# Kernel optimization log

Measured on AMD Instinct MI355X. Metric: run time of the kernel, lower is better.

Reference implementation:

```python
import jax, jax.numpy as jnp
import numpy as np

N_NODES = 100000
N_EDGES = 1600000
IN_FEAT = 128
HIDDEN = 64
OUT_EMB = 64
N_GRAPHS = 256
PD_EPS = 1e-6  # torch PairwiseDistance eps added to the difference


def gcn_conv(x, src, dst, W, b):
    """PyG GCNConv: h = x@W, add self-loops, sym-normalized scatter-add, + bias."""
    n = x.shape[0]
    h = x @ W  # [N, out]
    loops = jnp.arange(n)
    s = jnp.concatenate([src, loops])
    d = jnp.concatenate([dst, loops])
    deg = jnp.zeros((n,), h.dtype).at[d].add(1.0)
    dinv = jnp.where(deg > 0, jax.lax.rsqrt(jnp.maximum(deg, 1.0)), 0.0)
    norm = (dinv[s] * dinv[d])[:, None]  # [E+N, 1]
    out = jnp.zeros_like(h).at[d].add(norm * h[s])  # gather + scatter-add
    return out + b


def mean_pool(x, batch, num_graphs):
    s = jax.ops.segment_sum(x, batch, num_segments=num_graphs)
    cnt = jax.ops.segment_sum(jnp.ones((x.shape[0],), x.dtype), batch,
                              num_segments=num_graphs)
    return s / jnp.maximum(cnt, 1.0)[:, None]


def tower(x, edge_index, batch, params, num_graphs):
    W1, b1, W2, b2, W3, b3, Wlin, blin = params
    src, dst = edge_index[0], edge_index[1]
    x = jax.nn.relu(gcn_conv(x, src, dst, W1, b1))
    x = jax.nn.relu(gcn_conv(x, src, dst, W2, b2))
    x = gcn_conv(x, src, dst, W3, b3)
    x = mean_pool(x, batch, num_graphs)
    # dropout omitted for determinism (eval mode)
    return x @ Wlin + blin


def setup_inputs() -> dict:
    key = jax.random.key(0)
    ks = jax.random.split(key, 16)

    def glorot(k, fan_in, fan_out):
        lim = np.sqrt(6.0 / (fan_in + fan_out))
        return jax.random.uniform(k, (fan_in, fan_out), jnp.float32, -lim, lim)

    return {
        "x1": jax.random.normal(ks[0], (N_NODES, IN_FEAT), jnp.float32),
        "edge_index1": jax.random.randint(ks[1], (2, N_EDGES), 0, N_NODES),
        "batch1": jnp.sort(jax.random.randint(ks[2], (N_NODES,), 0, N_GRAPHS)),
        "x2": jax.random.normal(ks[3], (N_NODES, IN_FEAT), jnp.float32),
        "edge_index2": jax.random.randint(ks[4], (2, N_EDGES), 0, N_NODES),
        "batch2": jnp.sort(jax.random.randint(ks[5], (N_NODES,), 0, N_GRAPHS)),
        "W1": glorot(ks[6], IN_FEAT, HIDDEN),
        "b1": jnp.zeros((HIDDEN,), jnp.float32),
        "W2": glorot(ks[7], HIDDEN, HIDDEN),
        "b2": jnp.zeros((HIDDEN,), jnp.float32),
        "W3": glorot(ks[8], HIDDEN, HIDDEN),
        "b3": jnp.zeros((HIDDEN,), jnp.float32),
        "Wlin": glorot(ks[9], HIDDEN, OUT_EMB),
        "blin": jnp.zeros((OUT_EMB,), jnp.float32),
        "num_graphs": N_GRAPHS,
    }


def reference(x1, edge_index1, batch1, x2, edge_index2, batch2,
              W1, b1, W2, b2, W3, b3, Wlin, blin, num_graphs):
    params = (W1, b1, W2, b2, W3, b3, Wlin, blin)
    e1 = tower(x1, edge_index1, batch1, params, num_graphs)  # [G, OUT_EMB]
    e2 = tower(x2, edge_index2, batch2, params, num_graphs)
    diff = e1 - e2 + PD_EPS
    return jnp.sqrt(jnp.sum(diff * diff, axis=-1))  # L2 PairwiseDistance, [G]
```

## Files before the change

### kernel.cpp

```cpp
#include <hip/hip_runtime.h>
#include <hip/hip_bf16.h>
#include <math.h>

#define NGRAPHS 256
#define PD_EPS 1e-6f
#define POOL_CHUNK 64
#define NCOLOR 16
#define CSHIFT 4
#define KB 96

typedef __hip_bfloat16 bf16;
typedef unsigned short ushort_t;
typedef short bf8_t __attribute__((ext_vector_type(8)));
typedef float f4_t __attribute__((ext_vector_type(4)));

static __device__ __forceinline__ int wave_uniform(int v) {
  return __builtin_amdgcn_readfirstlane(v);
}
static __device__ __forceinline__ float b2f(bf16 h) { return __bfloat162float(h); }
static __device__ __forceinline__ bf16 f2b(float f) { return __float2bfloat16(f); }
static __device__ __forceinline__ short f2bbits(float f) {
  bf16 h = __float2bfloat16(f);
  return *reinterpret_cast<short*>(&h);
}

__global__ __launch_bounds__(256) void k_count_part(const int* __restrict__ dst,
                                                    ushort_t* __restrict__ partial,
                                                    int E, int n, int rng) {
  extern __shared__ int hist[];
  int color = blockIdx.x & (NCOLOR - 1);
  int sub = blockIdx.x >> CSHIFT;
  int base = color * rng;
  int hi = n - base; if (hi > rng) hi = rng;
  for (int i = threadIdx.x; i < rng; i += 256) hist[i] = 0;
  __syncthreads();
  const int stride = KB * 256;
  int e = sub * 256 + threadIdx.x;
  for (; e + 7 * stride < E; e += 8 * stride) {
    int d[8];
#pragma unroll
    for (int k = 0; k < 8; ++k) d[k] = dst[e + k * stride] - base;
#pragma unroll
    for (int k = 0; k < 8; ++k)
      if ((unsigned)d[k] < (unsigned)hi) atomicAdd(&hist[d[k]], 1);
  }
  for (; e < E; e += stride) {
    int d = dst[e] - base;
    if ((unsigned)d < (unsigned)hi) atomicAdd(&hist[d], 1);
  }
  __syncthreads();
  ushort_t* outp = partial + (size_t)blockIdx.x * rng;
  for (int i = threadIdx.x; i < rng; i += 256) outp[i] = (ushort_t)hist[i];
}

__global__ void k_reduce_part(ushort_t* __restrict__ partial, int* __restrict__ cnt,
                              float* __restrict__ dinv, int n, int rng) {
  int i = blockIdx.x * 256 + threadIdx.x;
  if (i >= n) return;
  int c = i / rng, li = i - c * rng;
  int acc = 0;
  for (int s = 0; s < KB; ++s) {
    size_t idx = (size_t)(s * NCOLOR + c) * rng + li;
    int t = partial[idx];
    partial[idx] = (ushort_t)acc;
    acc += t;
  }
  cnt[i] = acc;
  dinv[i] = 1.0f / sqrtf((float)(acc + 1));
}

__global__ void k_scan1(const int* __restrict__ cnt, int* __restrict__ off,
                        int* __restrict__ bsums, int n) {
  __shared__ int s[256];
  int tid = threadIdx.x;
  int gid = blockIdx.x * 256 + tid;
  int v = (gid < n) ? cnt[gid] : 0;
  s[tid] = v; __syncthreads();
  for (int o = 1; o < 256; o <<= 1) {
    int t = (tid >= o) ? s[tid - o] : 0;
    __syncthreads();
    s[tid] += t;
    __syncthreads();
  }
  if (gid < n) off[gid] = s[tid] - v;
  if (tid == 255) bsums[blockIdx.x] = s[255];
}

__global__ void k_scan2(int* __restrict__ bsums, int nb) {
  __shared__ int s[512];
  int tid = threadIdx.x;
  int v = (tid < nb) ? bsums[tid] : 0;
  s[tid] = v; __syncthreads();
  for (int o = 1; o < 512; o <<= 1) {
    int t = (tid >= o) ? s[tid - o] : 0;
    __syncthreads();
    s[tid] += t;
    __syncthreads();
  }
  if (tid < nb) bsums[tid] = s[tid] - v;
}

__global__ void k_off_final(int* __restrict__ off, const int* __restrict__ bsums,
                            int n, int E) {
  int gid = blockIdx.x * 256 + threadIdx.x;
  if (gid < n) off[gid] += bsums[blockIdx.x];
  if (gid == 0) off[n] = E;
}

__global__ __launch_bounds__(256) void k_fill_col(const int* __restrict__ src,
                                                  const int* __restrict__ dst,
                                                  const int* __restrict__ off,
                                                  const ushort_t* __restrict__ partial,
                                                  int* __restrict__ csr, int E, int n,
                                                  int rng) {
  extern __shared__ int cur[];
  int color = blockIdx.x & (NCOLOR - 1);
  int sub = blockIdx.x >> CSHIFT;
  int base = color * rng;
  int hi = n - base; if (hi > rng) hi = rng;
  const ushort_t* pp = partial + (size_t)blockIdx.x * rng;
  for (int i = threadIdx.x; i < hi; i += 256) cur[i] = off[base + i] + (int)pp[i];
  __syncthreads();
  const int stride = KB * 256;
  int e = sub * 256 + threadIdx.x;
  for (; e + 7 * stride < E; e += 8 * stride) {
    int d[8], s[8];
#pragma unroll
    for (int k = 0; k < 8; ++k) d[k] = dst[e + k * stride] - base;
#pragma unroll
    for (int k = 0; k < 8; ++k) s[k] = src[e + k * stride];
#pragma unroll
    for (int k = 0; k < 8; ++k) {
      if ((unsigned)d[k] < (unsigned)hi) {
        int p = atomicAdd(&cur[d[k]], 1);
        csr[p] = s[k];
      }
    }
  }
  for (; e < E; e += stride) {
    int d = dst[e] - base;
    if ((unsigned)d < (unsigned)hi) {
      int p = atomicAdd(&cur[d], 1);
      csr[p] = src[e];
    }
  }
}

template <int K, int INF32>
__global__ __launch_bounds__(256, 2) void k_gemm_mfma(const void* __restrict__ inv,
                                                      const float* __restrict__ Wg,
                                                      const float* __restrict__ dinv,
                                                      bf16* __restrict__ out, int n) {
  constexpr int KS = K / 32;
  int lane = threadIdx.x & 63;
  int quad = lane >> 4;
  int col = lane & 15;

  bf8_t bfrag[4][KS];
#pragma unroll
  for (int c = 0; c < 4; ++c)
#pragma unroll
    for (int s = 0; s < KS; ++s)
#pragma unroll
      for (int j = 0; j < 8; ++j)
        bfrag[c][s][j] = f2bbits(Wg[(s * 32 + quad * 8 + j) * 64 + c * 16 + col]);

  int wid = (blockIdx.x * blockDim.x + threadIdx.x) >> 6;
  int nw = (gridDim.x * blockDim.x) >> 6;
  int tiles = (n + 15) >> 4;
  for (int t = wid; t < tiles; t += nw) {
    int base = t << 4;
    int arow = base + col;
    if (arow >= n) arow = n - 1;

    bf8_t afrag[KS];
    if (INF32) {
      const float* xr = (const float*)inv + (size_t)arow * K;
#pragma unroll
      for (int s = 0; s < KS; ++s) {
        float4 u0 = *(const float4*)(xr + s * 32 + quad * 8);
        float4 u1 = *(const float4*)(xr + s * 32 + quad * 8 + 4);
        afrag[s][0] = f2bbits(u0.x);
        afrag[s][1] = f2bbits(u0.y);
        afrag[s][2] = f2bbits(u0.z);
        afrag[s][3] = f2bbits(u0.w);
        afrag[s][4] = f2bbits(u1.x);
        afrag[s][5] = f2bbits(u1.y);
        afrag[s][6] = f2bbits(u1.z);
        afrag[s][7] = f2bbits(u1.w);
      }
    } else {
      const bf16* xr = (const bf16*)inv + (size_t)arow * K;
#pragma unroll
      for (int s = 0; s < KS; ++s)
        afrag[s] = *(const bf8_t*)(xr + s * 32 + quad * 8);
    }

    f4_t acc[4];
#pragma unroll
    for (int c = 0; c < 4; ++c) acc[c] = (f4_t){0.f, 0.f, 0.f, 0.f};
#pragma unroll
    for (int s = 0; s < KS; ++s)
#pragma unroll
      for (int c = 0; c < 4; ++c)
        acc[c] = __builtin_amdgcn_mfma_f32_16x16x32_bf16(afrag[s], bfrag[c][s],
                                                         acc[c], 0, 0, 0);
#pragma unroll
    for (int r = 0; r < 4; ++r) {
      int row = base + quad * 4 + r;
      if (row < n) {
        float sc = dinv[row];
#pragma unroll
        for (int c = 0; c < 4; ++c)
          out[(size_t)row * 64 + c * 16 + col] = f2b(acc[c][r] * sc);
      }
    }
  }
}

template <int MODE>
__global__ __launch_bounds__(256) void k_agg(const bf16* __restrict__ hp,
                                             const int* __restrict__ off,
                                             const int* __restrict__ csr,
                                             const float* __restrict__ dinv,
                                             const float* __restrict__ bias,
                                             void* __restrict__ outv, int n) {
  int lane = threadIdx.x & 63;
  int wid = (blockIdx.x * blockDim.x + threadIdx.x) >> 6;
  int nw = (gridDim.x * blockDim.x) >> 6;
  float b = (MODE == 2) ? 0.f : bias[lane];
  for (int node = wid; node < n; node += nw) {
    int un = wave_uniform(node);
    int beg = off[un], end = off[un + 1];
    float acc = b2f(hp[(size_t)un * 64 + lane]);
    int e = beg;
    int efull = beg + ((end - beg) & ~7);
    for (; e < efull; e += 8) {
      int s0 = csr[e + 0], s1 = csr[e + 1], s2 = csr[e + 2], s3 = csr[e + 3];
      int s4 = csr[e + 4], s5 = csr[e + 5], s6 = csr[e + 6], s7 = csr[e + 7];
      float a0 = b2f(hp[(size_t)s0 * 64 + lane]);
      float a1 = b2f(hp[(size_t)s1 * 64 + lane]);
      float a2 = b2f(hp[(size_t)s2 * 64 + lane]);
      float a3 = b2f(hp[(size_t)s3 * 64 + lane]);
      float a4 = b2f(hp[(size_t)s4 * 64 + lane]);
      float a5 = b2f(hp[(size_t)s5 * 64 + lane]);
      float a6 = b2f(hp[(size_t)s6 * 64 + lane]);
      float a7 = b2f(hp[(size_t)s7 * 64 + lane]);
      acc += ((a0 + a1) + (a2 + a3)) + ((a4 + a5) + (a6 + a7));
    }
    int rem = end - e;
    if (rem & 4) {
      int s0 = csr[e + 0], s1 = csr[e + 1], s2 = csr[e + 2], s3 = csr[e + 3];
      float a0 = b2f(hp[(size_t)s0 * 64 + lane]);
      float a1 = b2f(hp[(size_t)s1 * 64 + lane]);
      float a2 = b2f(hp[(size_t)s2 * 64 + lane]);
      float a3 = b2f(hp[(size_t)s3 * 64 + lane]);
      acc += (a0 + a1) + (a2 + a3);
      e += 4;
    }
    if (rem & 2) {
      int s0 = csr[e + 0], s1 = csr[e + 1];
      float a0 = b2f(hp[(size_t)s0 * 64 + lane]);
      float a1 = b2f(hp[(size_t)s1 * 64 + lane]);
      acc += a0 + a1;
      e += 2;
    }
    if (rem & 1) {
      acc += b2f(hp[(size_t)csr[e] * 64 + lane]);
    }
    float di = dinv[un];
    if (MODE == 2) {
      ((float*)outv)[(size_t)un * 64 + lane] = acc * di;
    } else {
      float v = fmaf(acc, di, b);
      v = fmaxf(v, 0.f);
      if (MODE == 1) v *= di;
      ((bf16*)outv)[(size_t)un * 64 + lane] = f2b(v);
    }
  }
}

__global__ __launch_bounds__(256) void k_pool(const float* __restrict__ x3,
                                              const int* __restrict__ batch,
                                              float* __restrict__ pooled,
                                              float* __restrict__ cnt, int n) {
  int lane = threadIdx.x & 63;
  int wid = (blockIdx.x * blockDim.x + threadIdx.x) >> 6;
  int beg = wid * POOL_CHUNK;
  if (beg >= n) return;
  int end = beg + POOL_CHUNK;
  if (end > n) end = n;

  int cur = wave_uniform(batch[beg]);
  float acc = 0.f;
  int cl = 0;
  int i = beg;
  for (; i + 4 <= end; i += 4) {
    int g0 = wave_uniform(batch[i + 0]);
    int g3 = wave_uniform(batch[i + 3]);
    float a0 = x3[(size_t)(i + 0) * 64 + lane];
    float a1 = x3[(size_t)(i + 1) * 64 + lane];
    float a2 = x3[(size_t)(i + 2) * 64 + lane];
    float a3 = x3[(size_t)(i + 3) * 64 + lane];
    if (g0 == cur && g3 == cur) {
      acc += a0 + a1 + a2 + a3;
      cl += 4;
    } else {
      float av[4] = {a0, a1, a2, a3};
#pragma unroll
      for (int k = 0; k < 4; ++k) {
        int g = wave_uniform(batch[i + k]);
        if (g != cur) {
          atomicAdd(&pooled[cur * 64 + lane], acc);
          if (lane == 0) atomicAdd(&cnt[cur], (float)cl);
          acc = 0.f; cl = 0; cur = g;
        }
        acc += av[k];
        cl += 1;
      }
    }
  }
  for (; i < end; ++i) {
    int g = wave_uniform(batch[i]);
    float a = x3[(size_t)i * 64 + lane];
    if (g != cur) {
      atomicAdd(&pooled[cur * 64 + lane], acc);
      if (lane == 0) atomicAdd(&cnt[cur], (float)cl);
      acc = 0.f; cl = 0; cur = g;
    }
    acc += a;
    cl += 1;
  }
  atomicAdd(&pooled[cur * 64 + lane], acc);
  if (lane == 0) atomicAdd(&cnt[cur], (float)cl);
}

__global__ void k_final(const float* __restrict__ pooled1, const float* __restrict__ cnt1,
                        const float* __restrict__ pooled2, const float* __restrict__ cnt2,
                        const float* __restrict__ W3, const float* __restrict__ b3,
                        const float* __restrict__ Wlin, const float* __restrict__ blin,
                        float* __restrict__ outp) {
  int g = blockIdx.x;
  int lane = threadIdx.x;
  float c1 = fmaxf(cnt1[g], 1.f), c2 = fmaxf(cnt2[g], 1.f);
  float p1 = pooled1[g * 64 + lane] / c1;
  float p2 = pooled2[g * 64 + lane] / c2;
  float q1 = b3[lane], q2 = b3[lane];
  for (int j = 0; j < 64; ++j) {
    float w = W3[j * 64 + lane];
    q1 = fmaf(__shfl(p1, j), w, q1);
    q2 = fmaf(__shfl(p2, j), w, q2);
  }
  float e1 = blin[lane], e2 = blin[lane];
  for (int j = 0; j < 64; ++j) {
    float w = Wlin[j * 64 + lane];
    e1 = fmaf(__shfl(q1, j), w, e1);
    e2 = fmaf(__shfl(q2, j), w, e2);
  }
  float d = e1 - e2 + PD_EPS;
  float sq = d * d;
  for (int o = 32; o > 0; o >>= 1) sq += __shfl_down(sq, o);
  if (lane == 0) outp[g] = sqrtf(sq);
}

extern "C" void kernel_launch(void* const* d_in, const int* in_sizes, int n_in,
                              void* d_out, int out_size, void* d_ws, size_t ws_size,
                              hipStream_t stream) {
  const float* x1 = (const float*)d_in[0];
  const int* ei1 = (const int*)d_in[1];
  const int* batch1 = (const int*)d_in[2];
  const float* x2 = (const float*)d_in[3];
  const int* ei2 = (const int*)d_in[4];
  const int* batch2 = (const int*)d_in[5];
  const float* W1 = (const float*)d_in[6];
  const float* b1 = (const float*)d_in[7];
  const float* W2 = (const float*)d_in[8];
  const float* b2 = (const float*)d_in[9];
  const float* W3 = (const float*)d_in[10];
  const float* b3 = (const float*)d_in[11];
  const float* Wlin = (const float*)d_in[12];
  const float* blin = (const float*)d_in[13];

  const int N = in_sizes[2];
  const int E = in_sizes[1] / 2;
  const int rng = (N + NCOLOR - 1) / NCOLOR;

  char* p = (char*)d_ws;
  auto alloc = [&](size_t bytes) {
    char* r = p;
    p += (bytes + 255) & ~(size_t)255;
    return r;
  };
  int* off = (int*)alloc((size_t)(N + 1) * 4);
  int* cntn = (int*)alloc((size_t)N * 4);
  int* bsums = (int*)alloc(512 * 4);
  float* dinv = (float*)alloc((size_t)N * 4);
  int* csr = (int*)alloc((size_t)E * 4);
  char* unionbuf = alloc((size_t)N * 64 * 4);
  ushort_t* partial = (ushort_t*)unionbuf;
  float* bufF = (float*)unionbuf;
  bf16* hpA = (bf16*)alloc((size_t)N * 64 * 2);
  bf16* hpB = (bf16*)alloc((size_t)N * 64 * 2);
  float* pooled1 = (float*)alloc((size_t)NGRAPHS * 64 * 4);
  float* cnt1 = (float*)alloc((size_t)NGRAPHS * 4);
  float* pooled2 = (float*)alloc((size_t)NGRAPHS * 64 * 4);
  float* cnt2 = (float*)alloc((size_t)NGRAPHS * 4);
  size_t poolspan = (size_t)((char*)(cnt2 + NGRAPHS) - (char*)pooled1);

  const int nbN = (N + 255) / 256;
  const size_t ldsB = (size_t)rng * 4;

  hipMemsetAsync(pooled1, 0, poolspan, stream);

  for (int t = 0; t < 2; ++t) {
    const float* x = t ? x2 : x1;
    const int* src = t ? ei2 : ei1;
    const int* dst = src + E;
    const int* batch = t ? batch2 : batch1;
    float* pooled = t ? pooled2 : pooled1;
    float* cnt = t ? cnt2 : cnt1;

    k_count_part<<<NCOLOR * KB, 256, ldsB, stream>>>(dst, partial, E, N, rng);
    k_reduce_part<<<nbN, 256, 0, stream>>>(partial, cntn, dinv, N, rng);
    k_scan1<<<nbN, 256, 0, stream>>>(cntn, off, bsums, N);
    k_scan2<<<1, 512, 0, stream>>>(bsums, nbN);
    k_off_final<<<nbN, 256, 0, stream>>>(off, bsums, N, E);
    k_fill_col<<<NCOLOR * KB, 256, ldsB, stream>>>(src, dst, off, partial, csr, E, N,
                                                   rng);

    k_gemm_mfma<128, 1><<<512, 256, 0, stream>>>(x, W1, dinv, hpA, N);
    k_agg<0><<<2048, 256, 0, stream>>>(hpA, off, csr, dinv, b1, hpB, N);
    k_gemm_mfma<64, 0><<<512, 256, 0, stream>>>(hpB, W2, dinv, hpA, N);
    k_agg<1><<<2048, 256, 0, stream>>>(hpA, off, csr, dinv, b2, hpB, N);
    k_agg<2><<<2048, 256, 0, stream>>>(hpB, off, csr, dinv, b3, bufF, N);

    const int poolWaves = (N + POOL_CHUNK - 1) / POOL_CHUNK;
    k_pool<<<(poolWaves + 3) / 4, 256, 0, stream>>>(bufF, batch, pooled, cnt, N);
  }
  k_final<<<NGRAPHS, 64, 0, stream>>>(pooled1, cnt1, pooled2, cnt2, W3, b3, Wlin,
                                      blin, (float*)d_out);
}
```

Baseline: 580.6 us.

## Batch both towers into single kernel launches and fuse final aggregation with pooling

```diff
diff --git a/kernel.cpp b/kernel.cpp
--- a/kernel.cpp
+++ b/kernel.cpp
@@ -4,7 +4,6 @@
 
 #define NGRAPHS 256
 #define PD_EPS 1e-6f
-#define POOL_CHUNK 64
 #define NCOLOR 16
 #define CSHIFT 4
 #define KB 96
@@ -24,12 +23,19 @@
   return *reinterpret_cast<short*>(&h);
 }
 
-__global__ __launch_bounds__(256) void k_count_part(const int* __restrict__ dst,
-                                                    ushort_t* __restrict__ partial,
+__global__ __launch_bounds__(256) void k_count_part(const int* __restrict__ dst1,
+                                                    const int* __restrict__ dst2,
+                                                    ushort_t* __restrict__ partial1,
+                                                    ushort_t* __restrict__ partial2,
                                                     int E, int n, int rng) {
   extern __shared__ int hist[];
-  int color = blockIdx.x & (NCOLOR - 1);
-  int sub = blockIdx.x >> CSHIFT;
+  const int tbase = NCOLOR * KB;
+  int tower = blockIdx.x >= tbase;
+  int bid = blockIdx.x - (tower ? tbase : 0);
+  const int* dst = tower ? dst2 : dst1;
+  ushort_t* partial = tower ? partial2 : partial1;
+  int color = bid & (NCOLOR - 1);
+  int sub = bid >> CSHIFT;
   int base = color * rng;
   int hi = n - base; if (hi > rng) hi = rng;
   for (int i = threadIdx.x; i < rng; i += 256) hist[i] = 0;
@@ -49,32 +55,36 @@
     if ((unsigned)d < (unsigned)hi) atomicAdd(&hist[d], 1);
   }
   __syncthreads();
-  ushort_t* outp = partial + (size_t)blockIdx.x * rng;
+  ushort_t* outp = partial + (size_t)bid * rng;
   for (int i = threadIdx.x; i < rng; i += 256) outp[i] = (ushort_t)hist[i];
 }
 
-__global__ void k_reduce_part(ushort_t* __restrict__ partial, int* __restrict__ cnt,
-                              float* __restrict__ dinv, int n, int rng) {
-  int i = blockIdx.x * 256 + threadIdx.x;
-  if (i >= n) return;
-  int c = i / rng, li = i - c * rng;
+__global__ void k_reduce_part(ushort_t* __restrict__ partial1,
+                              ushort_t* __restrict__ partial2, int* __restrict__ cnt,
+                              float* __restrict__ dinv, int n, int npad, int rng) {
+  int gi = blockIdx.x * 256 + threadIdx.x;
+  int tower = gi >= npad;
+  int li = gi - (tower ? npad : 0);
+  if (li >= n) { cnt[gi] = 0; return; }
+  ushort_t* partial = tower ? partial2 : partial1;
+  int c = li / rng, lli = li - c * rng;
   int acc = 0;
   for (int s = 0; s < KB; ++s) {
-    size_t idx = (size_t)(s * NCOLOR + c) * rng + li;
+    size_t idx = (size_t)(s * NCOLOR + c) * rng + lli;
     int t = partial[idx];
     partial[idx] = (ushort_t)acc;
     acc += t;
   }
-  cnt[i] = acc;
-  dinv[i] = 1.0f / sqrtf((float)(acc + 1));
+  cnt[gi] = acc;
+  dinv[tower * n + li] = 1.0f / sqrtf((float)(acc + 1));
 }
 
 __global__ void k_scan1(const int* __restrict__ cnt, int* __restrict__ off,
-                        int* __restrict__ bsums, int n) {
+                        int* __restrict__ bsums, int n, int npad) {
   __shared__ int s[256];
   int tid = threadIdx.x;
   int gid = blockIdx.x * 256 + tid;
-  int v = (gid < n) ? cnt[gid] : 0;
+  int v = cnt[gid];
   s[tid] = v; __syncthreads();
   for (int o = 1; o < 256; o <<= 1) {
     int t = (tid >= o) ? s[tid - o] : 0;
@@ -82,44 +92,65 @@
     s[tid] += t;
     __syncthreads();
   }
-  if (gid < n) off[gid] = s[tid] - v;
+  int tower = gid >= npad;
+  int li = gid - (tower ? npad : 0);
+  if (li < n) off[tower * (n + 1) + li] = s[tid] - v;
   if (tid == 255) bsums[blockIdx.x] = s[255];
 }
 
-__global__ void k_scan2(int* __restrict__ bsums, int nb) {
-  __shared__ int s[512];
+__global__ void k_scan2(int* __restrict__ bsums, int nb, int segstart) {
+  __shared__ int s[1024];
+  __shared__ int seg0;
   int tid = threadIdx.x;
   int v = (tid < nb) ? bsums[tid] : 0;
   s[tid] = v; __syncthreads();
-  for (int o = 1; o < 512; o <<= 1) {
+  for (int o = 1; o < 1024; o <<= 1) {
     int t = (tid >= o) ? s[tid - o] : 0;
     __syncthreads();
     s[tid] += t;
     __syncthreads();
   }
-  if (tid < nb) bsums[tid] = s[tid] - v;
+  int excl = s[tid] - v;
+  if (tid == segstart) seg0 = excl;
+  __syncthreads();
+  if (tid < nb) bsums[tid] = (tid >= segstart) ? excl - seg0 : excl;
 }
 
 __global__ void k_off_final(int* __restrict__ off, const int* __restrict__ bsums,
-                            int n, int E) {
+                            int n, int npad, int E) {
   int gid = blockIdx.x * 256 + threadIdx.x;
-  if (gid < n) off[gid] += bsums[blockIdx.x];
-  if (gid == 0) off[n] = E;
-}
-
-__global__ __launch_bounds__(256) void k_fill_col(const int* __restrict__ src,
-                                                  const int* __restrict__ dst,
+  int tower = gid >= npad;
+  int li = gid - (tower ? npad : 0);
+  if (li < n) off[tower * (n + 1) + li] += bsums[blockIdx.x];
+  if (li == 0) off[tower * (n + 1) + n] = E;
+}
+
+__global__ __launch_bounds__(256) void k_fill_col(const int* __restrict__ src1,
+                                                  const int* __restrict__ dst1,
+                                                  const int* __restrict__ src2,
+                                                  const int* __restrict__ dst2,
                                                   const int* __restrict__ off,
-                                                  const ushort_t* __restrict__ partial,
+                                                  const ushort_t* __restrict__ partial1,
+                                                  const ushort_t* __restrict__ partial2,
                                                   int* __restrict__ csr, int E, int n,
                                                   int rng) {
   extern __shared__ int cur[];
-  int color = blockIdx.x & (NCOLOR - 1);
-  int sub = blockIdx.x >> CSHIFT;
+  const int tbase = NCOLOR * KB;
+  int tower = blockIdx.x >= tbase;
+  int bid = blockIdx.x - (tower ? tbase : 0);
+  const int* src = tower ? src2 : src1;
+  const int* dst = tower ? dst2 : dst1;
+  const ushort_t* partial = tower ? partial2 : partial1;
+  const int* offt = off + tower * (n + 1);
+  int cbase = tower ? E : 0;
+  int nodeoff = tower ? n : 0;
+  int color = bid & (NCOLOR - 1);
+  int sub = bid >> CSHIFT;
   int base = color * rng;
   int hi = n - base; if (hi > rng) hi = rng;
-  const ushort_t* pp = partial + (size_t)blockIdx.x * rng;
-  for (int i = threadIdx.x; i < hi; i += 256) cur[i] = off[base + i] + (int)pp[i];
+  const ushort_t* pp = partial + (size_t)bid * rng;
+  for (int i = threadIdx.x; i < hi; i += 256)
+    cur[i] = offt[base + i] + (int)pp[i] + cbase;
   __syncthreads();
   const int stride = KB * 256;
   int e = sub * 256 + threadIdx.x;
@@ -133,7 +164,7 @@
     for (int k = 0; k < 8; ++k) {
       if ((unsigned)d[k] < (unsigned)hi) {
         int p = atomicAdd(&cur[d[k]], 1);
-        csr[p] = s[k];
+        csr[p] = s[k] + nodeoff;
       }
     }
   }
@@ -141,16 +172,19 @@
     int d = dst[e] - base;
     if ((unsigned)d < (unsigned)hi) {
       int p = atomicAdd(&cur[d], 1);
-      csr[p] = src[e];
+      csr[p] = src[e] + nodeoff;
     }
   }
 }
 
 template <int K, int INF32>
-__global__ __launch_bounds__(256, 2) void k_gemm_mfma(const void* __restrict__ inv,
+__global__ __launch_bounds__(256, 2) void k_gemm_mfma(const float* __restrict__ xf1,
+                                                      const float* __restrict__ xf2,
+                                                      const bf16* __restrict__ xb,
                                                       const float* __restrict__ Wg,
                                                       const float* __restrict__ dinv,
-                                                      bf16* __restrict__ out, int n) {
+                                                      bf16* __restrict__ out, int n2,
+                                                      int nper) {
   constexpr int KS = K / 32;
   int lane = threadIdx.x & 63;
   int quad = lane >> 4;
@@ -167,15 +201,17 @@
 
   int wid = (blockIdx.x * blockDim.x + threadIdx.x) >> 6;
   int nw = (gridDim.x * blockDim.x) >> 6;
-  int tiles = (n + 15) >> 4;
+  int tiles = (n2 + 15) >> 4;
   for (int t = wid; t < tiles; t += nw) {
     int base = t << 4;
     int arow = base + col;
-    if (arow >= n) arow = n - 1;
+    if (arow >= n2) arow = n2 - 1;
 
     bf8_t afrag[KS];
     if (INF32) {
-      const float* xr = (const float*)inv + (size_t)arow * K;
+      int tower = arow >= nper;
+      const float* xr = (tower ? xf2 : xf1) +
+                        (size_t)(arow - (tower ? nper : 0)) * K;
 #pragma unroll
       for (int s = 0; s < KS; ++s) {
         float4 u0 = *(const float4*)(xr + s * 32 + quad * 8);
@@ -190,7 +226,7 @@
         afrag[s][7] = f2bbits(u1.w);
       }
     } else {
-      const bf16* xr = (const bf16*)inv + (size_t)arow * K;
+      const bf16* xr = xb + (size_t)arow * K;
 #pragma unroll
       for (int s = 0; s < KS; ++s)
         afrag[s] = *(const bf8_t*)(xr + s * 32 + quad * 8);
@@ -208,7 +244,7 @@
 #pragma unroll
     for (int r = 0; r < 4; ++r) {
       int row = base + quad * 4 + r;
-      if (row < n) {
+      if (row < n2) {
         float sc = dinv[row];
 #pragma unroll
         for (int c = 0; c < 4; ++c)
@@ -224,14 +260,19 @@
                                              const int* __restrict__ csr,
                                              const float* __restrict__ dinv,
                                              const float* __restrict__ bias,
-                                             void* __restrict__ outv, int n) {
+                                             bf16* __restrict__ outv, int n2,
+                                             int nper, int E) {
   int lane = threadIdx.x & 63;
   int wid = (blockIdx.x * blockDim.x + threadIdx.x) >> 6;
   int nw = (gridDim.x * blockDim.x) >> 6;
-  float b = (MODE == 2) ? 0.f : bias[lane];
-  for (int node = wid; node < n; node += nw) {
+  float b = bias[lane];
+  for (int node = wid; node < n2; node += nw) {
     int un = wave_uniform(node);
-    int beg = off[un], end = off[un + 1];
+    int tower = un >= nper;
+    int ln = un - (tower ? nper : 0);
+    const int* o = off + tower * (nper + 1);
+    int cb = tower ? E : 0;
+    int beg = o[ln] + cb, end = o[ln + 1] + cb;
     float acc = b2f(hp[(size_t)un * 64 + lane]);
     int e = beg;
     int efull = beg + ((end - beg) & ~7);
@@ -269,70 +310,78 @@
       acc += b2f(hp[(size_t)csr[e] * 64 + lane]);
     }
     float di = dinv[un];
-    if (MODE == 2) {
-      ((float*)outv)[(size_t)un * 64 + lane] = acc * di;
-    } else {
-      float v = fmaf(acc, di, b);
-      v = fmaxf(v, 0.f);
-      if (MODE == 1) v *= di;
-      ((bf16*)outv)[(size_t)un * 64 + lane] = f2b(v);
-    }
-  }
-}
-
-__global__ __launch_bounds__(256) void k_pool(const float* __restrict__ x3,
-                                              const int* __restrict__ batch,
-                                              float* __restrict__ pooled,
-                                              float* __restrict__ cnt, int n) {
+    float v = fmaf(acc, di, b);
+    v = fmaxf(v, 0.f);
+    if (MODE == 1) v *= di;
+    outv[(size_t)un * 64 + lane] = f2b(v);
+  }
+}
+
+__global__ __launch_bounds__(256) void k_agg_pool(const bf16* __restrict__ hp,
+                                                  const int* __restrict__ off,
+                                                  const int* __restrict__ csr,
+                                                  const float* __restrict__ dinv,
+                                                  const int* __restrict__ batch1,
+                                                  const int* __restrict__ batch2,
+                                                  float* __restrict__ pooled1,
+                                                  float* __restrict__ cnt1,
+                                                  float* __restrict__ pooled2,
+                                                  float* __restrict__ cnt2, int n2,
+                                                  int nper, int E) {
   int lane = threadIdx.x & 63;
   int wid = (blockIdx.x * blockDim.x + threadIdx.x) >> 6;
-  int beg = wid * POOL_CHUNK;
-  if (beg >= n) return;
-  int end = beg + POOL_CHUNK;
-  if (end > n) end = n;
-
-  int cur = wave_uniform(batch[beg]);
-  float acc = 0.f;
-  int cl = 0;
-  int i = beg;
-  for (; i + 4 <= end; i += 4) {
-    int g0 = wave_uniform(batch[i + 0]);
-    int g3 = wave_uniform(batch[i + 3]);
-    float a0 = x3[(size_t)(i + 0) * 64 + lane];
-    float a1 = x3[(size_t)(i + 1) * 64 + lane];
-    float a2 = x3[(size_t)(i + 2) * 64 + lane];
-    float a3 = x3[(size_t)(i + 3) * 64 + lane];
-    if (g0 == cur && g3 == cur) {
-      acc += a0 + a1 + a2 + a3;
-      cl += 4;
-    } else {
-      float av[4] = {a0, a1, a2, a3};
-#pragma unroll
-      for (int k = 0; k < 4; ++k) {
-        int g = wave_uniform(batch[i + k]);
-        if (g != cur) {
-          atomicAdd(&pooled[cur * 64 + lane], acc);
-          if (lane == 0) atomicAdd(&cnt[cur], (float)cl);
-          acc = 0.f; cl = 0; cur = g;
-        }
-        acc += av[k];
-        cl += 1;
-      }
-    }
-  }
-  for (; i < end; ++i) {
-    int g = wave_uniform(batch[i]);
-    float a = x3[(size_t)i * 64 + lane];
-    if (g != cur) {
-      atomicAdd(&pooled[cur * 64 + lane], acc);
-      if (lane == 0) atomicAdd(&cnt[cur], (float)cl);
-      acc = 0.f; cl = 0; cur = g;
-    }
-    acc += a;
-    cl += 1;
-  }
-  atomicAdd(&pooled[cur * 64 + lane], acc);
-  if (lane == 0) atomicAdd(&cnt[cur], (float)cl);
+  int nw = (gridDim.x * blockDim.x) >> 6;
+  for (int node = wid; node < n2; node += nw) {
+    int un = wave_uniform(node);
+    int tower = un >= nper;
+    int ln = un - (tower ? nper : 0);
+    const int* o = off + tower * (nper + 1);
+    int cb = tower ? E : 0;
+    int beg = o[ln] + cb, end = o[ln + 1] + cb;
+    float acc = b2f(hp[(size_t)un * 64 + lane]);
+    int e = beg;
+    int efull = beg + ((end - beg) & ~7);
+    for (; e < efull; e += 8) {
+      int s0 = csr[e + 0], s1 = csr[e + 1], s2 = csr[e + 2], s3 = csr[e + 3];
+      int s4 = csr[e + 4], s5 = csr[e + 5], s6 = csr[e + 6], s7 = csr[e + 7];
+      float a0 = b2f(hp[(size_t)s0 * 64 + lane]);
+      float a1 = b2f(hp[(size_t)s1 * 64 + lane]);
+      float a2 = b2f(hp[(size_t)s2 * 64 + lane]);
+      float a3 = b2f(hp[(size_t)s3 * 64 + lane]);
+      float a4 = b2f(hp[(size_t)s4 * 64 + lane]);
+      float a5 = b2f(hp[(size_t)s5 * 64 + lane]);
+      float a6 = b2f(hp[(size_t)s6 * 64 + lane]);
+      float a7 = b2f(hp[(size_t)s7 * 64 + lane]);
+      acc += ((a0 + a1) + (a2 + a3)) + ((a4 + a5) + (a6 + a7));
+    }
+    int rem = end - e;
+    if (rem & 4) {
+      int s0 = csr[e + 0], s1 = csr[e + 1], s2 = csr[e + 2], s3 = csr[e + 3];
+      float a0 = b2f(hp[(size_t)s0 * 64 + lane]);
+      float a1 = b2f(hp[(size_t)s1 * 64 + lane]);
+      float a2 = b2f(hp[(size_t)s2 * 64 + lane]);
+      float a3 = b2f(hp[(size_t)s3 * 64 + lane]);
+      acc += (a0 + a1) + (a2 + a3);
+      e += 4;
+    }
+    if (rem & 2) {
+      int s0 = csr[e + 0], s1 = csr[e + 1];
+      float a0 = b2f(hp[(size_t)s0 * 64 + lane]);
+      float a1 = b2f(hp[(size_t)s1 * 64 + lane]);
+      acc += a0 + a1;
+      e += 2;
+    }
+    if (rem & 1) {
+      acc += b2f(hp[(size_t)csr[e] * 64 + lane]);
+    }
+    float t = acc * dinv[un];
+    const int* batch = tower ? batch2 : batch1;
+    float* pooled = tower ? pooled2 : pooled1;
+    float* cntp = tower ? cnt2 : cnt1;
+    int g = batch[ln];
+    atomicAdd(&pooled[g * 64 + lane], t);
+    if (lane == 0) atomicAdd(&cntp[g], 1.0f);
+  }
 }
 
 __global__ void k_final(const float* __restrict__ pooled1, const float* __restrict__ cnt1,
@@ -384,6 +433,12 @@
   const int N = in_sizes[2];
   const int E = in_sizes[1] / 2;
   const int rng = (N + NCOLOR - 1) / NCOLOR;
+  const int nbN = (N + 255) / 256;
+  const int Npad = nbN * 256;
+  const int nb2 = 2 * nbN;
+
+  const int* src1 = ei1; const int* dst1 = ei1 + E;
+  const int* src2 = ei2; const int* dst2 = ei2 + E;
 
   char* p = (char*)d_ws;
   auto alloc = [&](size_t bytes) {
@@ -391,52 +446,47 @@
     p += (bytes + 255) & ~(size_t)255;
     return r;
   };
-  int* off = (int*)alloc((size_t)(N + 1) * 4);
-  int* cntn = (int*)alloc((size_t)N * 4);
-  int* bsums = (int*)alloc(512 * 4);
-  float* dinv = (float*)alloc((size_t)N * 4);
-  int* csr = (int*)alloc((size_t)E * 4);
-  char* unionbuf = alloc((size_t)N * 64 * 4);
-  ushort_t* partial = (ushort_t*)unionbuf;
-  float* bufF = (float*)unionbuf;
-  bf16* hpA = (bf16*)alloc((size_t)N * 64 * 2);
-  bf16* hpB = (bf16*)alloc((size_t)N * 64 * 2);
+  int* off = (int*)alloc((size_t)2 * (N + 1) * 4);
+  int* cntn = (int*)alloc((size_t)2 * Npad * 4);
+  int* bsums = (int*)alloc(1024 * 4);
+  float* dinv = (float*)alloc((size_t)2 * N * 4);
+  int* csr = (int*)alloc((size_t)2 * E * 4);
+  ushort_t* partial1 = (ushort_t*)alloc((size_t)NCOLOR * KB * rng * 2);
+  ushort_t* partial2 = (ushort_t*)alloc((size_t)NCOLOR * KB * rng * 2);
+  bf16* hpA = (bf16*)alloc((size_t)2 * N * 64 * 2);
+  bf16* hpB = (bf16*)alloc((size_t)2 * N * 64 * 2);
   float* pooled1 = (float*)alloc((size_t)NGRAPHS * 64 * 4);
   float* cnt1 = (float*)alloc((size_t)NGRAPHS * 4);
   float* pooled2 = (float*)alloc((size_t)NGRAPHS * 64 * 4);
   float* cnt2 = (float*)alloc((size_t)NGRAPHS * 4);
   size_t poolspan = (size_t)((char*)(cnt2 + NGRAPHS) - (char*)pooled1);
 
-  const int nbN = (N + 255) / 256;
   const size_t ldsB = (size_t)rng * 4;
+  const int N2 = 2 * N;
 
   hipMemsetAsync(pooled1, 0, poolspan, stream);
 
-  for (int t = 0; t < 2; ++t) {
-    const float* x = t ? x2 : x1;
-    const int* src = t ? ei2 : ei1;
-    const int* dst = src + E;
-    const int* batch = t ? batch2 : batch1;
-    float* pooled = t ? pooled2 : pooled1;
-    float* cnt = t ? cnt2 : cnt1;
-
-    k_count_part<<<NCOLOR * KB, 256, ldsB, stream>>>(dst, partial, E, N, rng);
-    k_reduce_part<<<nbN, 256, 0, stream>>>(partial, cntn, dinv, N, rng);
-    k_scan1<<<nbN, 256, 0, stream>>>(cntn, off, bsums, N);
-    k_scan2<<<1, 512, 0, stream>>>(bsums, nbN);
-    k_off_final<<<nbN, 256, 0, stream>>>(off, bsums, N, E);
-    k_fill_col<<<NCOLOR * KB, 256, ldsB, stream>>>(src, dst, off, partial, csr, E, N,
-                                                   rng);
-
-    k_gemm_mfma<128, 1><<<512, 256, 0, stream>>>(x, W1, dinv, hpA, N);
-    k_agg<0><<<2048, 256, 0, stream>>>(hpA, off, csr, dinv, b1, hpB, N);
-    k_gemm_mfma<64, 0><<<512, 256, 0, stream>>>(hpB, W2, dinv, hpA, N);
-    k_agg<1><<<2048, 256, 0, stream>>>(hpA, off, csr, dinv, b2, hpB, N);
-    k_agg<2><<<2048, 256, 0, stream>>>(hpB, off, csr, dinv, b3, bufF, N);
-
-    const int poolWaves = (N + POOL_CHUNK - 1) / POOL_CHUNK;
-    k_pool<<<(poolWaves + 3) / 4, 256, 0, stream>>>(bufF, batch, pooled, cnt, N);
-  }
+  k_count_part<<<2 * NCOLOR * KB, 256, ldsB, stream>>>(dst1, dst2, partial1,
+                                                       partial2, E, N, rng);
+  k_reduce_part<<<nb2, 256, 0, stream>>>(partial1, partial2, cntn, dinv, N, Npad,
+                                         rng);
+  k_scan1<<<nb2, 256, 0, stream>>>(cntn, off, bsums, N, Npad);
+  k_scan2<<<1, 1024, 0, stream>>>(bsums, nb2, nbN);
+  k_off_final<<<nb2, 256, 0, stream>>>(off, bsums, N, Npad, E);
+  k_fill_col<<<2 * NCOLOR * KB, 256, ldsB, stream>>>(src1, dst1, src2, dst2, off,
+                                                     partial1, partial2, csr, E, N,
+                                                     rng);
+
+  k_gemm_mfma<128, 1><<<1024, 256, 0, stream>>>(x1, x2, (const bf16*)nullptr, W1,
+                                                dinv, hpA, N2, N);
+  k_agg<0><<<4096, 256, 0, stream>>>(hpA, off, csr, dinv, b1, hpB, N2, N, E);
+  k_gemm_mfma<64, 0><<<1024, 256, 0, stream>>>((const float*)nullptr,
+                                               (const float*)nullptr, hpB, W2, dinv,
+                                               hpA, N2, N);
+  k_agg<1><<<4096, 256, 0, stream>>>(hpA, off, csr, dinv, b2, hpB, N2, N, E);
+  k_agg_pool<<<4096, 256, 0, stream>>>(hpB, off, csr, dinv, batch1, batch2, pooled1,
+                                       cnt1, pooled2, cnt2, N2, N, E);
+
   k_final<<<NGRAPHS, 64, 0, stream>>>(pooled1, cnt1, pooled2, cnt2, W3, b3, Wlin,
                                       blin, (float*)d_out);
 }
```

Result: slower. 938.9 us (+61.7%).
